# Kernel tuning notes

Hardware: AMD Instinct MI355X
Metric: run time of the kernel (lower is better)

The kernel has to match this reference:

```python
import jax, jax.numpy as jnp
import numpy as np

N = 20000    # nodes
F = 64       # channels (num_features)
Z = 10       # species
DEG = 16
E = N * DEG  # edges
RD = 8       # radial_dim
EPS = 0.25   # epsilon (avg-degree normalization)
SQRT3 = 3.0 ** 0.5


def setup_inputs() -> dict:
    key = jax.random.key(0)
    ks = jax.random.split(key, 22)
    g = lambda i, shape, s=1.0: jax.random.normal(ks[i], shape, jnp.float32) * s
    return dict(
        vectors=g(0, (E, 3)),
        node_s=g(1, (N, F)),
        node_v=g(2, (N, F, 3)),
        radial_embed=jax.random.uniform(ks[3], (E, RD), jnp.float32),
        senders=jax.random.randint(ks[4], (E,), 0, N),
        receivers=jax.random.randint(ks[5], (E,), 0, N),
        species_counts=jnp.full((Z,), N // Z, dtype=jnp.int32),
        Wup0=g(6, (F, F)), Wup1=g(7, (F, F)),
        R1=g(8, (RD, 64)), R2=g(9, (64, 64)), R3=g(10, (64, 64)), R4=g(11, (64, 4 * F)),
        Wd0=g(12, (F, F)), Wd1=g(13, (F, F)),
        Ws0=g(14, (Z, F, F)), Ws1=g(15, (Z, F, F)),
        Wsc=g(16, (Z, 9, F)), Proj=g(17, (9, 9), 1.0 / 3.0),
        Wl0=g(18, (F, F)), Wl1=g(19, (F, F)),
        Wr=g(20, (F, 1)),
    )


def _forward(vectors, node_s, node_v, radial_embed, senders, receivers,
             species_counts, Wup0, Wup1, R1, R2, R3, R4, Wd0, Wd1,
             Ws0, Ws1, Wsc, Proj, Wl0, Wl1, Wr):
    inv = 1.0 / np.sqrt(F)
    # species index per node (counts -> contiguous blocks), like jnp.repeat in SymmetricContraction
    sidx = jnp.repeat(jnp.arange(Z), species_counts, total_repeat_length=N)

    # spherical harmonics l=0 (constant 1, folded into weights) and l=1
    r = jnp.linalg.norm(vectors, axis=-1, keepdims=True)
    Y1 = SQRT3 * vectors / r                              # (E,3)

    # species-indexed skip connection on input feats
    skip_s = jnp.einsum('nf,nfg->ng', node_s, Ws0[sidx]) * inv
    skip_v = jnp.einsum('nfi,nfg->ngi', node_v, Ws1[sidx]) * inv

    # linear_up (per-irrep channel mixing)
    hs = (node_s @ Wup0) * inv                            # (N,F)
    hv = jnp.einsum('nfi,fg->ngi', node_v, Wup1) * inv    # (N,F,3)

    # radial MLP -> per-edge, per-path, per-channel TP weights (weight_numel = 4*F)
    a = jax.nn.silu(radial_embed @ R1)
    a = jax.nn.silu(a @ R2)
    a = jax.nn.silu(a @ R3)
    w = (a @ R4).reshape(E, 4, F)

    # channelwise tensor product: gather senders, 4 CG paths, scatter to receivers
    es = hs[senders]                                      # (E,F)
    ev = hv[senders]                                      # (E,F,3)
    m_s = w[:, 0] * es + w[:, 1] * (jnp.einsum('efi,ei->ef', ev, Y1) / SQRT3)
    m_v = w[:, 2][..., None] * ev + w[:, 3][..., None] * (es[..., None] * Y1[:, None, :]) / SQRT3
    hs = jax.ops.segment_sum(m_s, receivers, num_segments=N) * EPS
    hv = jax.ops.segment_sum(m_v, receivers, num_segments=N) * EPS

    # linear_down
    hs = (hs @ Wd0) * inv
    hv = jnp.einsum('nfi,fg->ngi', hv, Wd1) * inv

    # symmetric contraction (correlation 1..3), species-keyed weights through fixed projection
    wsc = jnp.einsum('zpu,pb->zbu', Wsc, Proj)[sidx]      # (N,9,F)
    vv = jnp.sum(hv * hv, -1)                             # (N,F)
    bs = jnp.stack([hs, hs * hs, vv, hs ** 3, hs * vv], axis=1)                    # (N,5,F)
    bv = jnp.stack([hv, hs[..., None] * hv, (hs * hs)[..., None] * hv,
                    vv[..., None] * hv], axis=1)                                   # (N,4,F,3)
    cs = jnp.einsum('nbf,nbf->nf', bs, wsc[:, :5])
    cv = jnp.einsum('nbfi,nbf->nfi', bv, wsc[:, 5:])

    # linear_sc
    cs = (cs @ Wl0) * inv
    cv = jnp.einsum('nfi,fg->ngi', cv, Wl1) * inv

    # add skip
    h_s = cs + skip_s
    h_v = cv + skip_v

    # readout (0e -> 1x0e; only scalars participate)
    out = (h_s @ Wr) * inv                                # (N,1)
    return out, h_s, h_v


def reference(vectors, node_s, node_v, radial_embed, senders, receivers,
              species_counts, Wup0, Wup1, R1, R2, R3, R4, Wd0, Wd1,
              Ws0, Ws1, Wsc, Proj, Wl0, Wl1, Wr):
    return _forward(vectors, node_s, node_v, radial_embed, senders, receivers,
                    species_counts, Wup0, Wup1, R1, R2, R3, R4, Wd0, Wd1,
                    Ws0, Ws1, Wsc, Proj, Wl0, Wl1, Wr)
```

## Files before the change

kernel.cpp:

```cpp
#include <hip/hip_runtime.h>
#include <hip/hip_bf16.h>
#include <hip/hip_fp16.h>
#include <math.h>

#define N_NODES 20000
#define FCH 64
#define ZSP 10
#define E_EDGES 320000
#define RDIM 8
#define EPSC 0.25f
#define SQRT3C 1.7320508075688772f
#define INV_SQRT3C 0.57735026918962576f
#define INV_F 0.125f

#define OFF_EUP    0
#define OFF_SKS    (N_NODES*128)
#define OFF_SKV    (OFF_SKS + N_NODES*64)
#define OFF_HSMID  (OFF_SKV + N_NODES*192)
#define OFF_HVMID  (OFF_HSMID + N_NODES*64)
#define OFF_WSCP   (OFF_HVMID + N_NODES*192)
#define OFF_FRAGS  (OFF_WSCP + ZSP*576)
#define OFF_WBUF   (OFF_FRAGS + 13312)
#define OFF_CSR    (OFF_WBUF + E_EDGES*128)
#define OFF_WF     (OFF_CSR + E_EDGES*4 + 360132)
#define CSR_CNT    0
#define CSR_PTR    20000
#define CSR_SEID   40001
#define CSR_AUX    360001

#define SU_WSC   5760
#define SU_PREP  (SU_WSC + 3328)
#define SU_PREP2 (SU_PREP + 26624)
#define SU_HIST  (SU_PREP2 + E_EDGES)

typedef __attribute__((ext_vector_type(8))) short bhalf8;
typedef __attribute__((ext_vector_type(4))) float f32x4;

__device__ __forceinline__ float silu_f(float x) {
    float e = __builtin_amdgcn_exp2f(x * -1.442695040888963f);
    return x * __builtin_amdgcn_rcpf(1.0f + e);
}

__device__ __forceinline__ unsigned short f2bf(float x) {
    unsigned int u = __float_as_uint(x);
    unsigned int r = u + 0x7FFFu + ((u >> 16) & 1u);
    return (unsigned short)(r >> 16);
}

__device__ __forceinline__ unsigned int pack_bf2(float lo, float hi) {
    __hip_bfloat162 b = __float22bfloat162_rn(make_float2(lo, hi));
    return *(unsigned int*)&b;
}

__device__ __forceinline__ unsigned int pack_h2(float lo, float hi) {
    __half2 h = __floats2half2_rn(lo, hi);
    return *(unsigned int*)&h;
}

__device__ __forceinline__ bhalf8 mk8(unsigned a, unsigned b, unsigned c, unsigned d) {
    uint4 u; u.x = a; u.y = b; u.z = c; u.w = d;
    return *(bhalf8*)&u;
}

__device__ __forceinline__ float half_lo(unsigned v) {
    return __half2float(__ushort_as_half((unsigned short)(v & 0xFFFFu)));
}
__device__ __forceinline__ float half_hi(unsigned v) {
    return __half2float(__ushort_as_half((unsigned short)(v >> 16)));
}

__device__ __forceinline__ void split_f32(float x, short& h, short& l) {
    unsigned int u = __float_as_uint(x);
    unsigned int hb = u & 0xFFFF0000u;
    h = (short)(u >> 16);
    float r = x - __uint_as_float(hb);
    l = (short)(__float_as_uint(r) >> 16);
}

__device__ __forceinline__ int species_of(int n, const int* counts) {
    int acc = 0, s = ZSP - 1;
#pragma unroll
    for (int z = 0; z < ZSP; z++) {
        int c = counts[z];
        if (n >= acc && n < acc + c) s = z;
        acc += c;
    }
    return s;
}

__global__ __launch_bounds__(256) void k_setup(
    const float* __restrict__ Wsc, const float* __restrict__ Proj, float* __restrict__ wscp,
    const float* __restrict__ R1, const float* __restrict__ R2,
    const float* __restrict__ R3, const float* __restrict__ R4,
    unsigned short* __restrict__ frags,
    const float* __restrict__ Wup0, const float* __restrict__ Wup1,
    const float* __restrict__ Ws0, const float* __restrict__ Ws1,
    const float* __restrict__ Wd0, const float* __restrict__ Wd1,
    const float* __restrict__ Wl0, const float* __restrict__ Wl1,
    unsigned short* __restrict__ wf,
    const int* __restrict__ receivers, int* __restrict__ csr) {
    int gid = blockIdx.x * 256 + threadIdx.x;
    if (gid < SU_WSC) {
        int z = gid / 576, t = gid % 576;
        int b = t >> 6, u = t & 63;
        float acc = 0.f;
#pragma unroll
        for (int p = 0; p < 9; p++) acc += Wsc[z * 576 + p * 64 + u] * Proj[p * 9 + b];
        wscp[z * 576 + b * 64 + u] = acc;
    } else if (gid < SU_PREP) {
        int id = gid - SU_WSC;
        int lane = id & 63, fi = id >> 6;
        int quad = lane >> 4, l15 = lane & 15;
        const float* W;
        int s, t, N;
        bool r1 = false;
        if (fi < 4)       { W = R1; s = 0; t = fi; N = 64; r1 = true; }
        else if (fi < 12) { W = R2; int x = fi - 4;  s = x >> 2; t = x & 3;  N = 64; }
        else if (fi < 20) { W = R3; int x = fi - 12; s = x >> 2; t = x & 3;  N = 64; }
        else              { W = R4; int x = fi - 20; s = x >> 4; t = x & 15; N = 256; }
        unsigned int v[4];
#pragma unroll
        for (int jj = 0; jj < 4; jj++) {
            unsigned short pk2[2];
#pragma unroll
            for (int o = 0; o < 2; o++) {
                int j = jj * 2 + o;
                int k = s * 32 + quad * 8 + j, n = t * 16 + l15;
                float val = (r1 && k >= RDIM) ? 0.f : W[k * N + n];
                pk2[o] = f2bf(val);
            }
            v[jj] = (unsigned int)pk2[0] | ((unsigned int)pk2[1] << 16);
        }
        uint4 pk; pk.x = v[0]; pk.y = v[1]; pk.z = v[2]; pk.w = v[3];
        ((uint4*)frags)[id] = pk;
    } else if (gid < SU_PREP2) {
        int id = gid - SU_PREP;
        int lane = id & 63, slot = id >> 6;
        int t = slot & 3, s = (slot >> 2) & 1, part = (slot >> 3) & 1, mat = slot >> 4;
        int quad = lane >> 4, l15 = lane & 15;
        const float* W;
        if (mat == 0)       W = Wup0;
        else if (mat == 1)  W = Wup1;
        else if (mat < 12)  W = Ws0 + (mat - 2) * 4096;
        else if (mat < 22)  W = Ws1 + (mat - 12) * 4096;
        else if (mat == 22) W = Wd0;
        else if (mat == 23) W = Wd1;
        else if (mat == 24) W = Wl0;
        else                W = Wl1;
        unsigned int v[4];
#pragma unroll
        for (int jj = 0; jj < 4; jj++) {
            unsigned short pk2[2];
#pragma unroll
            for (int o = 0; o < 2; o++) {
                int j = jj * 2 + o;
                int k = s * 32 + quad * 8 + j, n = t * 16 + l15;
                float x = W[k * 64 + n];
                short h, l;
                split_f32(x, h, l);
                pk2[o] = part == 0 ? (unsigned short)h : (unsigned short)l;
            }
            v[jj] = (unsigned int)pk2[0] | ((unsigned int)pk2[1] << 16);
        }
        uint4 pk; pk.x = v[0]; pk.y = v[1]; pk.z = v[2]; pk.w = v[3];
        ((uint4*)wf)[id] = pk;
    } else if (gid < SU_HIST) {
        int e = gid - SU_PREP2;
        atomicAdd(&csr[CSR_CNT + receivers[e]], 1);
    }
}

__global__ __launch_bounds__(256) void k_scan1(int* __restrict__ csr) {
    __shared__ int sb[256];
    int b = blockIdx.x, t = threadIdx.x;
    int i = b * 256 + t;
    int x = (i < N_NODES) ? csr[CSR_CNT + i] : 0;
    sb[t] = x;
    __syncthreads();
#pragma unroll
    for (int off = 1; off < 256; off <<= 1) {
        int v = (t >= off) ? sb[t - off] : 0;
        __syncthreads();
        sb[t] += v;
        __syncthreads();
    }
    if (i < N_NODES) csr[CSR_PTR + i] = sb[t] - x;
    if (t == 255) csr[CSR_AUX + b] = sb[255];
}

__global__ __launch_bounds__(128) void k_scan2(int* __restrict__ csr) {
    __shared__ int sb[128];
    int t = threadIdx.x;
    int x = (t < 79) ? csr[CSR_AUX + t] : 0;
    sb[t] = x;
    __syncthreads();
#pragma unroll
    for (int off = 1; off < 128; off <<= 1) {
        int v = (t >= off) ? sb[t - off] : 0;
        __syncthreads();
        sb[t] += v;
        __syncthreads();
    }
    csr[CSR_AUX + t] = sb[t] - x;
    if (t == 127) csr[CSR_PTR + N_NODES] = sb[127];
}

__global__ __launch_bounds__(256) void k_scan3(int* __restrict__ csr) {
    int b = blockIdx.x, t = threadIdx.x;
    int i = b * 256 + t;
    if (i >= N_NODES) return;
    int v = csr[CSR_PTR + i] + csr[CSR_AUX + b];
    csr[CSR_PTR + i] = v;
    csr[CSR_CNT + i] = v;
}

__global__ __launch_bounds__(256) void k_pre_bucket(
    const float* __restrict__ ns, const float* __restrict__ nv,
    const int* __restrict__ counts, const unsigned short* __restrict__ wf,
    const float* __restrict__ vectors, const int* __restrict__ senders,
    const int* __restrict__ receivers, int* __restrict__ csr,
    float4* __restrict__ erec, float* __restrict__ ws) {
    __shared__ uint2 eup_t[16][64];
    int tid = threadIdx.x;
    if (blockIdx.x >= 1250) {
        int e = (blockIdx.x - 1250) * 256 + tid;
        int pos = atomicAdd(&csr[CSR_CNT + receivers[e]], 1);
        float v0 = vectors[e * 3 + 0], v1 = vectors[e * 3 + 1], v2 = vectors[e * 3 + 2];
        float s = SQRT3C * rsqrtf(v0 * v0 + v1 * v1 + v2 * v2);
        csr[CSR_SEID + pos] = e;
        float4 r;
        r.x = v0 * s; r.y = v1 * s; r.z = v2 * s; r.w = __int_as_float(senders[e]);
        erec[pos] = r;
        return;
    }
    int w = tid >> 6, lane = tid & 63;
    int q = lane >> 4, l15 = lane & 15;
    int nw = blockIdx.x * 16;
    int sid = species_of(nw, counts);
    const f32x4 z4 = {0.f, 0.f, 0.f, 0.f};

    bhalf8 Ah[2], Al[2];
    if (w == 0) {
#pragma unroll
        for (int s = 0; s < 2; s++) {
            const float* rp = ns + (size_t)(nw + l15) * 64 + s * 32 + q * 8;
            float4 a = *(const float4*)rp, b = *(const float4*)(rp + 4);
            float x[8] = {a.x, a.y, a.z, a.w, b.x, b.y, b.z, b.w};
#pragma unroll
            for (int j = 0; j < 8; j++) { short h, l; split_f32(x[j], h, l); Ah[s][j] = h; Al[s][j] = l; }
        }
    } else {
        int i = w - 1;
#pragma unroll
        for (int s = 0; s < 2; s++) {
            const float* rp = nv + (size_t)(nw + l15) * 192 + i;
#pragma unroll
            for (int j = 0; j < 8; j++) {
                float x = rp[(s * 32 + q * 8 + j) * 3];
                short h, l; split_f32(x, h, l); Ah[s][j] = h; Al[s][j] = l;
            }
        }
    }

    const bhalf8* wfv = (const bhalf8*)wf;
    float* sks = ws + OFF_SKS;
    float* skv = ws + OFF_SKV;

    {
        int mat = (w == 0) ? 0 : 1;
#pragma unroll
        for (int t = 0; t < 4; t++) {
            f32x4 acc = z4;
#pragma unroll
            for (int s = 0; s < 2; s++) {
                bhalf8 bh = wfv[(size_t)(mat * 16 + 0 + s * 4 + t) * 64 + lane];
                bhalf8 bl = wfv[(size_t)(mat * 16 + 8 + s * 4 + t) * 64 + lane];
                acc = __builtin_amdgcn_mfma_f32_16x16x32_bf16(Ah[s], bh, acc, 0, 0, 0);
                acc = __builtin_amdgcn_mfma_f32_16x16x32_bf16(Al[s], bh, acc, 0, 0, 0);
                acc = __builtin_amdgcn_mfma_f32_16x16x32_bf16(Ah[s], bl, acc, 0, 0, 0);
            }
#pragma unroll
            for (int r = 0; r < 4; r++) {
                unsigned short us = __half_as_ushort(__float2half_rn(acc[r] * INV_F));
                ((unsigned short*)&eup_t[q * 4 + r][t * 16 + l15])[w] = us;
            }
        }
    }
    {
        int mat = (w == 0) ? 2 + sid : 12 + sid;
        float* dst = (w == 0) ? sks : skv;
        int stride = (w == 0) ? 64 : 192;
        int off = (w == 0) ? 0 : (w - 1) * 64;
#pragma unroll
        for (int t = 0; t < 4; t++) {
            f32x4 acc = z4;
#pragma unroll
            for (int s = 0; s < 2; s++) {
                bhalf8 bh = wfv[(size_t)(mat * 16 + 0 + s * 4 + t) * 64 + lane];
                bhalf8 bl = wfv[(size_t)(mat * 16 + 8 + s * 4 + t) * 64 + lane];
                acc = __builtin_amdgcn_mfma_f32_16x16x32_bf16(Ah[s], bh, acc, 0, 0, 0);
                acc = __builtin_amdgcn_mfma_f32_16x16x32_bf16(Al[s], bh, acc, 0, 0, 0);
                acc = __builtin_amdgcn_mfma_f32_16x16x32_bf16(Ah[s], bl, acc, 0, 0, 0);
            }
#pragma unroll
            for (int r = 0; r < 4; r++)
                dst[(size_t)(nw + q * 4 + r) * stride + off + t * 16 + l15] = acc[r] * INV_F;
        }
    }
    __syncthreads();
    uint2* eup = (uint2*)(ws + OFF_EUP);
    for (int k = tid; k < 1024; k += 256) {
        int n = k >> 6, f = k & 63;
        eup[(size_t)(nw + n) * 64 + f] = eup_t[n][f];
    }
}

template<int S>
__device__ __forceinline__ bhalf8 xfrag(const unsigned* pkA, const unsigned* pkB,
                                        int q, int l15) {
    int L0 = ((q & 1) << 5) + l15;
    int L1 = L0 + 16;
    bool hi = (q >> 1) != 0;
    unsigned a0 = (unsigned)__shfl((int)pkA[2 * S], L0, 64);
    unsigned a1 = (unsigned)__shfl((int)pkA[2 * S + 1], L0, 64);
    unsigned b0 = (unsigned)__shfl((int)pkB[2 * S], L0, 64);
    unsigned b1 = (unsigned)__shfl((int)pkB[2 * S + 1], L0, 64);
    unsigned c0 = (unsigned)__shfl((int)pkA[2 * S], L1, 64);
    unsigned c1 = (unsigned)__shfl((int)pkA[2 * S + 1], L1, 64);
    unsigned e0 = (unsigned)__shfl((int)pkB[2 * S], L1, 64);
    unsigned e1 = (unsigned)__shfl((int)pkB[2 * S + 1], L1, 64);
    return mk8(hi ? a1 : a0, hi ? b1 : b0, hi ? c1 : c0, hi ? e1 : e0);
}

__global__ __launch_bounds__(256) void k_mlp(
    const float* __restrict__ radial, const unsigned short* __restrict__ frags,
    const int* __restrict__ csr, unsigned short* __restrict__ wbuf) {
    __shared__ unsigned short r4lds[16384];
    int tid = threadIdx.x;
    int lane = tid & 63, w = tid >> 6, quad = lane >> 4, l15 = lane & 15;

    const uint4* r4g = (const uint4*)(frags + 20 * 64 * 8);
    uint4* r4l = (uint4*)r4lds;
    for (int i = tid; i < 2048; i += 256) r4l[i] = r4g[i];
    const bhalf8* fr = (const bhalf8*)frags;
    bhalf8 r1f[4], r2f[2][4], r3f[2][4];
#pragma unroll
    for (int t = 0; t < 4; t++) r1f[t] = fr[t * 64 + lane];
#pragma unroll
    for (int s = 0; s < 2; s++)
#pragma unroll
        for (int t = 0; t < 4; t++) {
            r2f[s][t] = fr[(4 + s * 4 + t) * 64 + lane];
            r3f[s][t] = fr[(12 + s * 4 + t) * 64 + lane];
        }
    __syncthreads();

    const f32x4 z4 = {0.f, 0.f, 0.f, 0.f};
    const bhalf8* r4f = (const bhalf8*)r4lds;

    int el0 = (blockIdx.x * 4 + w) * 16;

    bhalf8 af = {0, 0, 0, 0, 0, 0, 0, 0};
    if (quad == 0) {
        int eid = csr[CSR_SEID + el0 + l15];
        const float* rp = radial + (size_t)eid * 8;
        float4 ra = *(const float4*)rp;
        float4 rb = *(const float4*)(rp + 4);
        af[0] = (short)f2bf(ra.x); af[1] = (short)f2bf(ra.y);
        af[2] = (short)f2bf(ra.z); af[3] = (short)f2bf(ra.w);
        af[4] = (short)f2bf(rb.x); af[5] = (short)f2bf(rb.y);
        af[6] = (short)f2bf(rb.z); af[7] = (short)f2bf(rb.w);
    }
    unsigned pkA[4], pkB[4];
    {
        f32x4 acc[4];
#pragma unroll
        for (int t = 0; t < 4; t++)
            acc[t] = __builtin_amdgcn_mfma_f32_16x16x32_bf16(r1f[t], af, z4, 0, 0, 0);
#pragma unroll
        for (int t = 0; t < 4; t++) {
            pkA[t] = pack_bf2(silu_f(acc[t][0]), silu_f(acc[t][1]));
            pkB[t] = pack_bf2(silu_f(acc[t][2]), silu_f(acc[t][3]));
        }
    }
#pragma unroll
    for (int layer = 0; layer < 2; layer++) {
        bhalf8 b0 = xfrag<0>(pkA, pkB, quad, l15);
        bhalf8 b1 = xfrag<1>(pkA, pkB, quad, l15);
        f32x4 acc[4];
#pragma unroll
        for (int t = 0; t < 4; t++) {
            bhalf8 w0 = layer == 0 ? r2f[0][t] : r3f[0][t];
            bhalf8 w1 = layer == 0 ? r2f[1][t] : r3f[1][t];
            acc[t] = __builtin_amdgcn_mfma_f32_16x16x32_bf16(
                w1, b1, __builtin_amdgcn_mfma_f32_16x16x32_bf16(w0, b0, z4, 0, 0, 0), 0, 0, 0);
        }
#pragma unroll
        for (int t = 0; t < 4; t++) {
            pkA[t] = pack_bf2(silu_f(acc[t][0]), silu_f(acc[t][1]));
            pkB[t] = pack_bf2(silu_f(acc[t][2]), silu_f(acc[t][3]));
        }
    }
    {
        bhalf8 a0 = xfrag<0>(pkA, pkB, quad, l15);
        bhalf8 a1 = xfrag<1>(pkA, pkB, quad, l15);
#pragma unroll
        for (int t4 = 0; t4 < 4; t4++) {
            f32x4 p0 = __builtin_amdgcn_mfma_f32_16x16x32_bf16(
                a1, r4f[(16 + t4) * 64 + lane],
                __builtin_amdgcn_mfma_f32_16x16x32_bf16(a0, r4f[t4 * 64 + lane], z4, 0, 0, 0), 0, 0, 0);
            f32x4 p1 = __builtin_amdgcn_mfma_f32_16x16x32_bf16(
                a1, r4f[(20 + t4) * 64 + lane],
                __builtin_amdgcn_mfma_f32_16x16x32_bf16(a0, r4f[(4 + t4) * 64 + lane], z4, 0, 0, 0), 0, 0, 0);
            f32x4 p2 = __builtin_amdgcn_mfma_f32_16x16x32_bf16(
                a1, r4f[(24 + t4) * 64 + lane],
                __builtin_amdgcn_mfma_f32_16x16x32_bf16(a0, r4f[(8 + t4) * 64 + lane], z4, 0, 0, 0), 0, 0, 0);
            f32x4 p3 = __builtin_amdgcn_mfma_f32_16x16x32_bf16(
                a1, r4f[(28 + t4) * 64 + lane],
                __builtin_amdgcn_mfma_f32_16x16x32_bf16(a0, r4f[(12 + t4) * 64 + lane], z4, 0, 0, 0), 0, 0, 0);
#pragma unroll
            for (int r = 0; r < 4; r++) {
                int el = el0 + quad * 4 + r;
                int f = t4 * 16 + l15;
                uint2 pk;
                pk.x = pack_h2(p0[r], p1[r]);
                pk.y = pack_h2(p2[r], p3[r]);
                ((uint2*)wbuf)[(size_t)el * 64 + f] = pk;
            }
        }
    }
}

__global__ __launch_bounds__(256) void k_tp_gather(
    const unsigned short* __restrict__ wbuf, const int* __restrict__ csr,
    const float4* __restrict__ erec, float* __restrict__ ws) {
    int tid = threadIdx.x, w = tid >> 6, f = tid & 63;
    int n = blockIdx.x * 4 + w;
    const uint2* eup = (const uint2*)(ws + OFF_EUP);
    float* hs_mid = ws + OFF_HSMID;
    float* hv_mid = ws + OFF_HVMID;
    int beg = csr[CSR_PTR + n], end = csr[CSR_PTR + n + 1];
    float ams = 0.f, am0 = 0.f, am1 = 0.f, am2 = 0.f;

    if (beg < end) {
        int last = end - 1;
        float4 rcA = erec[beg];
        uint2 wrA = ((const uint2*)wbuf)[(size_t)beg * 64 + f];
        uint2 evA = eup[(size_t)__float_as_int(rcA.w) * 64 + f];
        int j1 = (beg + 1 < end) ? beg + 1 : last;
        float4 rcB = erec[j1];
        uint2 wrB = ((const uint2*)wbuf)[(size_t)j1 * 64 + f];
        uint2 evB = eup[(size_t)__float_as_int(rcB.w) * 64 + f];

        for (int i = beg; i < end; i++) {
            int j2 = (i + 2 < end) ? i + 2 : last;
            float4 rcC = erec[j2];
            uint2 wrC = ((const uint2*)wbuf)[(size_t)j2 * 64 + f];
            uint2 evC = eup[(size_t)__float_as_int(rcC.w) * 64 + f];
            float esA = half_lo(evA.x), eA0 = half_hi(evA.x);
            float eA1 = half_lo(evA.y), eA2 = half_hi(evA.y);
            float w0 = half_lo(wrA.x), w1 = half_hi(wrA.x);
            float w2 = half_lo(wrA.y), w3 = half_hi(wrA.y);
            float dot = eA0 * rcA.x + eA1 * rcA.y + eA2 * rcA.z;
            ams += w0 * esA + w1 * dot * INV_SQRT3C;
            float t3 = w3 * esA * INV_SQRT3C;
            am0 += w2 * eA0 + t3 * rcA.x;
            am1 += w2 * eA1 + t3 * rcA.y;
            am2 += w2 * eA2 + t3 * rcA.z;
            rcA = rcB; wrA = wrB; evA = evB;
            rcB = rcC; wrB = wrC; evB = evC;
        }
    }
    hs_mid[n * 64 + f] = ams * EPSC;
    hv_mid[n * 192 + f] = am0 * EPSC;
    hv_mid[n * 192 + 64 + f] = am1 * EPSC;
    hv_mid[n * 192 + 128 + f] = am2 * EPSC;
}

__global__ __launch_bounds__(256) void k_node_post(
    const int* __restrict__ counts, const unsigned short* __restrict__ wf,
    const float* __restrict__ Wr, float* __restrict__ ws, float* __restrict__ out) {
    __shared__ float T[4][16][68];
    int tid = threadIdx.x, w = tid >> 6, lane = tid & 63;
    int q = lane >> 4, l15 = lane & 15;
    int nw = blockIdx.x * 16;
    int sid = species_of(nw, counts);
    const f32x4 z4 = {0.f, 0.f, 0.f, 0.f};
    const bhalf8* wfv = (const bhalf8*)wf;
    const float* hs_mid = ws + OFF_HSMID;
    const float* hv_mid = ws + OFF_HVMID;
    const float* sks = ws + OFF_SKS;
    const float* skv = ws + OFF_SKV;
    const float* wscp = ws + OFF_WSCP;

    {
        const float* src = (w == 0) ? hs_mid + (size_t)nw * 64
                                    : hv_mid + (size_t)nw * 192 + (w - 1) * 64;
        int rstride = (w == 0) ? 64 : 192;
        bhalf8 Ah[2], Al[2];
#pragma unroll
        for (int s = 0; s < 2; s++) {
            const float* rp = src + (size_t)l15 * rstride + s * 32 + q * 8;
            float4 a = *(const float4*)rp, b = *(const float4*)(rp + 4);
            float x[8] = {a.x, a.y, a.z, a.w, b.x, b.y, b.z, b.w};
#pragma unroll
            for (int j = 0; j < 8; j++) { short h, l; split_f32(x[j], h, l); Ah[s][j] = h; Al[s][j] = l; }
        }
        int mat = (w == 0) ? 22 : 23;
#pragma unroll
        for (int t = 0; t < 4; t++) {
            f32x4 acc = z4;
#pragma unroll
            for (int s = 0; s < 2; s++) {
                bhalf8 bh = wfv[(size_t)(mat * 16 + 0 + s * 4 + t) * 64 + lane];
                bhalf8 bl = wfv[(size_t)(mat * 16 + 8 + s * 4 + t) * 64 + lane];
                acc = __builtin_amdgcn_mfma_f32_16x16x32_bf16(Ah[s], bh, acc, 0, 0, 0);
                acc = __builtin_amdgcn_mfma_f32_16x16x32_bf16(Al[s], bh, acc, 0, 0, 0);
                acc = __builtin_amdgcn_mfma_f32_16x16x32_bf16(Ah[s], bl, acc, 0, 0, 0);
            }
#pragma unroll
            for (int r = 0; r < 4; r++)
                T[w][q * 4 + r][t * 16 + l15] = acc[r] * INV_F;
        }
    }
    __syncthreads();

    {
        int col = tid & 63, rg = tid >> 6;
        float wv[9];
#pragma unroll
        for (int b = 0; b < 9; b++) wv[b] = wscp[sid * 576 + b * 64 + col];
#pragma unroll
        for (int rr = 0; rr < 4; rr++) {
            int row = rg * 4 + rr;
            float hs = T[0][row][col];
            float h0 = T[1][row][col], h1 = T[2][row][col], h2 = T[3][row][col];
            float vv = h0 * h0 + h1 * h1 + h2 * h2;
            float cs = wv[0] * hs + wv[1] * hs * hs + wv[2] * vv
                     + wv[3] * hs * hs * hs + wv[4] * hs * vv;
            float fv = wv[5] + wv[6] * hs + wv[7] * hs * hs + wv[8] * vv;
            T[0][row][col] = cs;
            T[1][row][col] = h0 * fv;
            T[2][row][col] = h1 * fv;
            T[3][row][col] = h2 * fv;
        }
    }
    __syncthreads();

    {
        bhalf8 Ah[2], Al[2];
#pragma unroll
        for (int s = 0; s < 2; s++) {
            const float* rp = &T[w][l15][s * 32 + q * 8];
            float4 a = *(const float4*)rp, b = *(const float4*)(rp + 4);
            float x[8] = {a.x, a.y, a.z, a.w, b.x, b.y, b.z, b.w};
#pragma unroll
            for (int j = 0; j < 8; j++) { short h, l; split_f32(x[j], h, l); Ah[s][j] = h; Al[s][j] = l; }
        }
        int mat = (w == 0) ? 24 : 25;
        float* d_hs = out + N_NODES;
        float* d_hv = out + N_NODES + N_NODES * 64;
        float p[4] = {0.f, 0.f, 0.f, 0.f};
#pragma unroll
        for (int t = 0; t < 4; t++) {
            f32x4 acc = z4;
#pragma unroll
            for (int s = 0; s < 2; s++) {
                bhalf8 bh = wfv[(size_t)(mat * 16 + 0 + s * 4 + t) * 64 + lane];
                bhalf8 bl = wfv[(size_t)(mat * 16 + 8 + s * 4 + t) * 64 + lane];
                acc = __builtin_amdgcn_mfma_f32_16x16x32_bf16(Ah[s], bh, acc, 0, 0, 0);
                acc = __builtin_amdgcn_mfma_f32_16x16x32_bf16(Al[s], bh, acc, 0, 0, 0);
                acc = __builtin_amdgcn_mfma_f32_16x16x32_bf16(Ah[s], bl, acc, 0, 0, 0);
            }
            int col = t * 16 + l15;
            if (w == 0) {
                float wr = Wr[col];
#pragma unroll
                for (int r = 0; r < 4; r++) {
                    int gn = nw + q * 4 + r;
                    float v = acc[r] * INV_F + sks[(size_t)gn * 64 + col];
                    d_hs[(size_t)gn * 64 + col] = v;
                    p[r] += v * wr;
                }
            } else {
                int i = w - 1;
#pragma unroll
                for (int r = 0; r < 4; r++) {
                    int gn = nw + q * 4 + r;
                    float v = acc[r] * INV_F + skv[(size_t)gn * 192 + i * 64 + col];
                    d_hv[(size_t)gn * 192 + col * 3 + i] = v;
                }
            }
        }
        if (w == 0) {
#pragma unroll
            for (int r = 0; r < 4; r++) {
#pragma unroll
                for (int off = 1; off < 16; off <<= 1) p[r] += __shfl_xor(p[r], off, 64);
                if (l15 == 0) out[nw + q * 4 + r] = p[r] * INV_F;
            }
        }
    }
}

extern "C" void kernel_launch(void* const* d_in, const int* in_sizes, int n_in,
                              void* d_out, int out_size, void* d_ws, size_t ws_size,
                              hipStream_t stream) {
    const float* vectors   = (const float*)d_in[0];
    const float* node_s    = (const float*)d_in[1];
    const float* node_v    = (const float*)d_in[2];
    const float* radial    = (const float*)d_in[3];
    const int*   senders   = (const int*)d_in[4];
    const int*   receivers = (const int*)d_in[5];
    const int*   counts    = (const int*)d_in[6];
    const float* Wup0 = (const float*)d_in[7];
    const float* Wup1 = (const float*)d_in[8];
    const float* R1   = (const float*)d_in[9];
    const float* R2   = (const float*)d_in[10];
    const float* R3   = (const float*)d_in[11];
    const float* R4   = (const float*)d_in[12];
    const float* Wd0  = (const float*)d_in[13];
    const float* Wd1  = (const float*)d_in[14];
    const float* Ws0  = (const float*)d_in[15];
    const float* Ws1  = (const float*)d_in[16];
    const float* Wsc  = (const float*)d_in[17];
    const float* Proj = (const float*)d_in[18];
    const float* Wl0  = (const float*)d_in[19];
    const float* Wl1  = (const float*)d_in[20];
    const float* Wr   = (const float*)d_in[21];
    float* ws  = (float*)d_ws;
    float* out = (float*)d_out;
    unsigned short* frags = (unsigned short*)(ws + OFF_FRAGS);
    unsigned short* wbuf  = (unsigned short*)(ws + OFF_WBUF);
    float4* erec = (float4*)(ws + OFF_CSR);
    int* csr = (int*)(ws + OFF_CSR + (size_t)E_EDGES * 4);
    unsigned short* wf = (unsigned short*)(ws + OFF_WF);

    hipMemsetAsync(csr + CSR_CNT, 0, N_NODES * sizeof(int), stream);
    k_setup<<<(SU_HIST + 255) / 256, 256, 0, stream>>>(
        Wsc, Proj, ws + OFF_WSCP, R1, R2, R3, R4, frags,
        Wup0, Wup1, Ws0, Ws1, Wd0, Wd1, Wl0, Wl1, wf, receivers, csr);
    k_scan1<<<79, 256, 0, stream>>>(csr);
    k_scan2<<<1, 128, 0, stream>>>(csr);
    k_scan3<<<79, 256, 0, stream>>>(csr);
    k_pre_bucket<<<2500, 256, 0, stream>>>(node_s, node_v, counts, wf,
                                           vectors, senders, receivers, csr, erec, ws);
    k_mlp<<<5000, 256, 0, stream>>>(radial, frags, csr, wbuf);
    k_tp_gather<<<N_NODES / 4, 256, 0, stream>>>(wbuf, csr, erec, ws);
    k_node_post<<<N_NODES / 16, 256, 0, stream>>>(counts, wf, Wr, ws, out);
}
```

Before: 301.5 us.

## Fuse per-edge tensor-product messages into MLP kernel and single-block scan

Moves the per-edge message computation (sender feature gather from eup, Y1 dot products, path weighting) out of the gather loop and into the radial MLP epilogue, so wbuf stores finished fp16 messages. The gather kernel then only sums contiguous messages per receiver and no longer does random eup/erec loads. It also replaces the three-kernel CSR prefix scan with a single 1024-thread block using wave shuffles, cutting two launches. The trade-off is that the random sender gathers now sit in the MFMA kernel, and messages are rounded to fp16 before accumulation.

```diff
diff --git a/kernel.cpp b/kernel.cpp
--- a/kernel.cpp
+++ b/kernel.cpp
@@ -26,7 +26,6 @@
 #define CSR_CNT    0
 #define CSR_PTR    20000
 #define CSR_SEID   40001
-#define CSR_AUX    360001
 
 #define SU_WSC   5760
 #define SU_PREP  (SU_WSC + 3328)
@@ -170,48 +169,44 @@
     }
 }
 
-__global__ __launch_bounds__(256) void k_scan1(int* __restrict__ csr) {
-    __shared__ int sb[256];
-    int b = blockIdx.x, t = threadIdx.x;
-    int i = b * 256 + t;
-    int x = (i < N_NODES) ? csr[CSR_CNT + i] : 0;
-    sb[t] = x;
-    __syncthreads();
-#pragma unroll
-    for (int off = 1; off < 256; off <<= 1) {
-        int v = (t >= off) ? sb[t - off] : 0;
+__global__ __launch_bounds__(1024) void k_scan_all(int* __restrict__ csr) {
+    __shared__ int wsum[16];
+    __shared__ int carry;
+    int t = threadIdx.x, lane = t & 63, wv = t >> 6;
+    int running = 0;
+    for (int i0 = 0; i0 < N_NODES; i0 += 1024) {
+        int i = i0 + t;
+        int x = (i < N_NODES) ? csr[CSR_CNT + i] : 0;
+        int s = x;
+#pragma unroll
+        for (int off = 1; off < 64; off <<= 1) {
+            int v = __shfl_up(s, off, 64);
+            if (lane >= off) s += v;
+        }
+        if (lane == 63) wsum[wv] = s;
         __syncthreads();
-        sb[t] += v;
+        if (wv == 0 && lane < 16) {
+            int v = wsum[lane];
+            int sc = v;
+#pragma unroll
+            for (int off = 1; off < 16; off <<= 1) {
+                int u = __shfl_up(sc, off, 64);
+                if (lane >= off) sc += u;
+            }
+            wsum[lane] = sc - v;
+            if (lane == 15) carry = sc;
+        }
         __syncthreads();
-    }
-    if (i < N_NODES) csr[CSR_PTR + i] = sb[t] - x;
-    if (t == 255) csr[CSR_AUX + b] = sb[255];
-}
-
-__global__ __launch_bounds__(128) void k_scan2(int* __restrict__ csr) {
-    __shared__ int sb[128];
-    int t = threadIdx.x;
-    int x = (t < 79) ? csr[CSR_AUX + t] : 0;
-    sb[t] = x;
-    __syncthreads();
-#pragma unroll
-    for (int off = 1; off < 128; off <<= 1) {
-        int v = (t >= off) ? sb[t - off] : 0;
+        int excl = s - x + wsum[wv];
+        if (i < N_NODES) {
+            int val = running + excl;
+            csr[CSR_PTR + i] = val;
+            csr[CSR_CNT + i] = val;
+        }
+        running += carry;
         __syncthreads();
-        sb[t] += v;
-        __syncthreads();
-    }
-    csr[CSR_AUX + t] = sb[t] - x;
-    if (t == 127) csr[CSR_PTR + N_NODES] = sb[127];
-}
-
-__global__ __launch_bounds__(256) void k_scan3(int* __restrict__ csr) {
-    int b = blockIdx.x, t = threadIdx.x;
-    int i = b * 256 + t;
-    if (i >= N_NODES) return;
-    int v = csr[CSR_PTR + i] + csr[CSR_AUX + b];
-    csr[CSR_PTR + i] = v;
-    csr[CSR_CNT + i] = v;
+    }
+    if (t == 0) csr[CSR_PTR + N_NODES] = running;
 }
 
 __global__ __launch_bounds__(256) void k_pre_bucket(
@@ -334,7 +329,8 @@
 
 __global__ __launch_bounds__(256) void k_mlp(
     const float* __restrict__ radial, const unsigned short* __restrict__ frags,
-    const int* __restrict__ csr, unsigned short* __restrict__ wbuf) {
+    const int* __restrict__ csr, const float4* __restrict__ erec,
+    unsigned short* __restrict__ wbuf, const float* __restrict__ ws) {
     __shared__ unsigned short r4lds[16384];
     int tid = threadIdx.x;
     int lane = tid & 63, w = tid >> 6, quad = lane >> 4, l15 = lane & 15;
@@ -357,6 +353,7 @@
 
     const f32x4 z4 = {0.f, 0.f, 0.f, 0.f};
     const bhalf8* r4f = (const bhalf8*)r4lds;
+    const uint2* eup = (const uint2*)(ws + OFF_EUP);
 
     int el0 = (blockIdx.x * 4 + w) * 16;
 
@@ -404,8 +401,20 @@
     {
         bhalf8 a0 = xfrag<0>(pkA, pkB, quad, l15);
         bhalf8 a1 = xfrag<1>(pkA, pkB, quad, l15);
+        float4 rc[4];
+        int sx[4];
+#pragma unroll
+        for (int r = 0; r < 4; r++) {
+            rc[r] = erec[el0 + quad * 4 + r];
+            sx[r] = __float_as_int(rc[r].w);
+        }
 #pragma unroll
         for (int t4 = 0; t4 < 4; t4++) {
+            int f = t4 * 16 + l15;
+            uint2 ev[4];
+#pragma unroll
+            for (int r = 0; r < 4; r++)
+                ev[r] = eup[(size_t)sx[r] * 64 + f];
             f32x4 p0 = __builtin_amdgcn_mfma_f32_16x16x32_bf16(
                 a1, r4f[(16 + t4) * 64 + lane],
                 __builtin_amdgcn_mfma_f32_16x16x32_bf16(a0, r4f[t4 * 64 + lane], z4, 0, 0, 0), 0, 0, 0);
@@ -420,11 +429,18 @@
                 __builtin_amdgcn_mfma_f32_16x16x32_bf16(a0, r4f[(12 + t4) * 64 + lane], z4, 0, 0, 0), 0, 0, 0);
 #pragma unroll
             for (int r = 0; r < 4; r++) {
+                float es = half_lo(ev[r].x), e0 = half_hi(ev[r].x);
+                float e1 = half_lo(ev[r].y), e2 = half_hi(ev[r].y);
+                float dot = e0 * rc[r].x + e1 * rc[r].y + e2 * rc[r].z;
+                float ms = p0[r] * es + p1[r] * dot * INV_SQRT3C;
+                float t3 = p3[r] * es * INV_SQRT3C;
+                float m0 = p2[r] * e0 + t3 * rc[r].x;
+                float m1 = p2[r] * e1 + t3 * rc[r].y;
+                float m2 = p2[r] * e2 + t3 * rc[r].z;
                 int el = el0 + quad * 4 + r;
-                int f = t4 * 16 + l15;
                 uint2 pk;
-                pk.x = pack_h2(p0[r], p1[r]);
-                pk.y = pack_h2(p2[r], p3[r]);
+                pk.x = pack_h2(ms, m0);
+                pk.y = pack_h2(m1, m2);
                 ((uint2*)wbuf)[(size_t)el * 64 + f] = pk;
             }
         }
@@ -433,42 +449,22 @@
 
 __global__ __launch_bounds__(256) void k_tp_gather(
     const unsigned short* __restrict__ wbuf, const int* __restrict__ csr,
-    const float4* __restrict__ erec, float* __restrict__ ws) {
+    float* __restrict__ ws) {
     int tid = threadIdx.x, w = tid >> 6, f = tid & 63;
     int n = blockIdx.x * 4 + w;
-    const uint2* eup = (const uint2*)(ws + OFF_EUP);
     float* hs_mid = ws + OFF_HSMID;
     float* hv_mid = ws + OFF_HVMID;
     int beg = csr[CSR_PTR + n], end = csr[CSR_PTR + n + 1];
     float ams = 0.f, am0 = 0.f, am1 = 0.f, am2 = 0.f;
-
     if (beg < end) {
         int last = end - 1;
-        float4 rcA = erec[beg];
-        uint2 wrA = ((const uint2*)wbuf)[(size_t)beg * 64 + f];
-        uint2 evA = eup[(size_t)__float_as_int(rcA.w) * 64 + f];
-        int j1 = (beg + 1 < end) ? beg + 1 : last;
-        float4 rcB = erec[j1];
-        uint2 wrB = ((const uint2*)wbuf)[(size_t)j1 * 64 + f];
-        uint2 evB = eup[(size_t)__float_as_int(rcB.w) * 64 + f];
-
+        uint2 mA = ((const uint2*)wbuf)[(size_t)beg * 64 + f];
         for (int i = beg; i < end; i++) {
-            int j2 = (i + 2 < end) ? i + 2 : last;
-            float4 rcC = erec[j2];
-            uint2 wrC = ((const uint2*)wbuf)[(size_t)j2 * 64 + f];
-            uint2 evC = eup[(size_t)__float_as_int(rcC.w) * 64 + f];
-            float esA = half_lo(evA.x), eA0 = half_hi(evA.x);
-            float eA1 = half_lo(evA.y), eA2 = half_hi(evA.y);
-            float w0 = half_lo(wrA.x), w1 = half_hi(wrA.x);
-            float w2 = half_lo(wrA.y), w3 = half_hi(wrA.y);
-            float dot = eA0 * rcA.x + eA1 * rcA.y + eA2 * rcA.z;
-            ams += w0 * esA + w1 * dot * INV_SQRT3C;
-            float t3 = w3 * esA * INV_SQRT3C;
-            am0 += w2 * eA0 + t3 * rcA.x;
-            am1 += w2 * eA1 + t3 * rcA.y;
-            am2 += w2 * eA2 + t3 * rcA.z;
-            rcA = rcB; wrA = wrB; evA = evB;
-            rcB = rcC; wrB = wrC; evB = evC;
+            int j1 = (i + 1 < end) ? i + 1 : last;
+            uint2 mB = ((const uint2*)wbuf)[(size_t)j1 * 64 + f];
+            ams += half_lo(mA.x); am0 += half_hi(mA.x);
+            am1 += half_lo(mA.y); am2 += half_hi(mA.y);
+            mA = mB;
         }
     }
     hs_mid[n * 64 + f] = ams * EPSC;
@@ -640,12 +636,10 @@
     k_setup<<<(SU_HIST + 255) / 256, 256, 0, stream>>>(
         Wsc, Proj, ws + OFF_WSCP, R1, R2, R3, R4, frags,
         Wup0, Wup1, Ws0, Ws1, Wd0, Wd1, Wl0, Wl1, wf, receivers, csr);
-    k_scan1<<<79, 256, 0, stream>>>(csr);
-    k_scan2<<<1, 128, 0, stream>>>(csr);
-    k_scan3<<<79, 256, 0, stream>>>(csr);
+    k_scan_all<<<1, 1024, 0, stream>>>(csr);
     k_pre_bucket<<<2500, 256, 0, stream>>>(node_s, node_v, counts, wf,
                                            vectors, senders, receivers, csr, erec, ws);
-    k_mlp<<<5000, 256, 0, stream>>>(radial, frags, csr, wbuf);
-    k_tp_gather<<<N_NODES / 4, 256, 0, stream>>>(wbuf, csr, erec, ws);
+    k_mlp<<<5000, 256, 0, stream>>>(radial, frags, csr, erec, wbuf, ws);
+    k_tp_gather<<<N_NODES / 4, 256, 0, stream>>>(wbuf, csr, ws);
     k_node_post<<<N_NODES / 16, 256, 0, stream>>>(counts, wf, Wr, ws, out);
 }
```

After: 300.5 us. Within noise of the previous version (-0.3%).
